# Performance work log

Measured on AMD Instinct MI355X. Metric: run time of the kernel, lower is better.

The kernel has to match this reference:

```python
import jax, jax.numpy as jnp
import numpy as np

SEQ = 32
D = 32  # d_model == GRU hidden size


def _gru_scan(gates_x, w_hh, b_hh):
    """gates_x: [S, B, 3H] precomputed input projections (r,z,n order, PyTorch convention).
    Returns outputs [S, B, H]."""
    H = w_hh.shape[1]
    B = gates_x.shape[1]

    def step(h, gx):
        gh = h @ w_hh.T + b_hh  # [B, 3H]
        r = jax.nn.sigmoid(gx[:, :H] + gh[:, :H])
        z = jax.nn.sigmoid(gx[:, H:2 * H] + gh[:, H:2 * H])
        n = jnp.tanh(gx[:, 2 * H:] + r * gh[:, 2 * H:])
        h_new = (1.0 - z) * n + z * h
        return h_new, h_new

    h0 = jnp.zeros((B, H), gates_x.dtype)
    _, ys = jax.lax.scan(step, h0, gates_x)
    return ys


def setup_inputs() -> dict:
    key = jax.random.key(0)
    ks = jax.random.split(key, 16)
    s = 0.1
    inp = {
        "x": jax.random.normal(ks[0], (32768, SEQ), dtype=jnp.float32),
        # feature extractor: Linear(1,16) -> LeakyReLU -> Linear(16,32)
        "w1": jax.random.normal(ks[1], (16, 1), dtype=jnp.float32) * s,
        "b1": jax.random.normal(ks[2], (16,), dtype=jnp.float32) * s,
        "w2": jax.random.normal(ks[3], (D, 16), dtype=jnp.float32) * s,
        "b2": jax.random.normal(ks[4], (D,), dtype=jnp.float32) * s,
        # GRU forward direction (PyTorch layout: [3H, in], gates r,z,n)
        "w_ih_f": jax.random.normal(ks[5], (3 * D, D), dtype=jnp.float32) * s,
        "w_hh_f": jax.random.normal(ks[6], (3 * D, D), dtype=jnp.float32) * s,
        "b_ih_f": jax.random.normal(ks[7], (3 * D,), dtype=jnp.float32) * s,
        "b_hh_f": jax.random.normal(ks[8], (3 * D,), dtype=jnp.float32) * s,
        # GRU backward direction
        "w_ih_b": jax.random.normal(ks[9], (3 * D, D), dtype=jnp.float32) * s,
        "w_hh_b": jax.random.normal(ks[10], (3 * D, D), dtype=jnp.float32) * s,
        "b_ih_b": jax.random.normal(ks[11], (3 * D,), dtype=jnp.float32) * s,
        "b_hh_b": jax.random.normal(ks[12], (3 * D,), dtype=jnp.float32) * s,
        # decoder: Linear(2*D, 128)
        "w_dec": jax.random.normal(ks[13], (128, 2 * D), dtype=jnp.float32) * s,
        "b_dec": jax.random.normal(ks[14], (128,), dtype=jnp.float32) * s,
    }
    return inp


def reference(x, w1, b1, w2, b2,
              w_ih_f, w_hh_f, b_ih_f, b_hh_f,
              w_ih_b, w_hh_b, b_ih_b, b_hh_b,
              w_dec, b_dec):
    x = x.reshape(-1, SEQ, 1)                      # [B, S, 1]
    h = jax.nn.leaky_relu(x @ w1.T + b1, 0.01)     # [B, S, 16]
    feat = h @ w2.T + b2                           # [B, S, D]

    # forward direction
    gx_f = jnp.einsum('bsd,gd->sbg', feat, w_ih_f) + b_ih_f  # [S, B, 3D]
    out_f = _gru_scan(gx_f, w_hh_f, b_hh_f)                  # [S, B, D]

    # backward direction: scan over time-reversed input, flip outputs back
    feat_rev = feat[:, ::-1, :]
    gx_b = jnp.einsum('bsd,gd->sbg', feat_rev, w_ih_b) + b_ih_b
    out_b = _gru_scan(gx_b, w_hh_b, b_hh_b)[::-1]            # [S, B, D]

    out = jnp.concatenate([out_f, out_b], axis=-1)  # [S, B, 2D]
    pooled = out.mean(axis=0)                       # [B, 2D]
    return pooled @ w_dec.T + b_dec                 # [B, 128]
```

## Files before the change

### kernel.cpp

```cpp
#include <hip/hip_runtime.h>


#define SEQB 32
#define NH   16
#define DH   32

typedef __attribute__((ext_vector_type(4))) float f32x4;
typedef __attribute__((ext_vector_type(8))) short s16x8;
typedef __attribute__((ext_vector_type(4))) unsigned int u32x4;

#define MFMA_B16(a, b, c) __builtin_amdgcn_mfma_f32_16x16x32_bf16((a), (b), (c), 0, 0, 0)

#define OFF_AHI  0u
#define OFF_ALO  12288u
#define OFF_AGX  24576u
#define OFF_ADEC 36864u
#define OFF_WC   53248u
#define OFF_BC   65536u

__device__ __forceinline__ unsigned short bf16_rne(float x) {
    unsigned u = __float_as_uint(x);
    return (unsigned short)((u + 0x7fffu + ((u >> 16) & 1u)) >> 16);
}
__device__ __forceinline__ unsigned pack_hi(unsigned a, unsigned b) {
    return __builtin_amdgcn_perm(a, b, 0x07060302u);
}
__device__ __forceinline__ int kperm(int q, int e) {
    return (e < 4) ? (4 * q + e) : (4 * q + 12 + e);
}

__global__ __launch_bounds__(1024) void gru_precompute_kernel(
    const float* __restrict__ w_ih_f, const float* __restrict__ b_ih_f,
    const float* __restrict__ w_ih_b, const float* __restrict__ b_ih_b,
    const float* __restrict__ w2, const float* __restrict__ b2,
    const float* __restrict__ whh_f, const float* __restrict__ whh_b,
    const float* __restrict__ bhh_f, const float* __restrict__ bhh_b,
    const float* __restrict__ w_dec,
    unsigned char* __restrict__ ws)
{
    const int t = threadIdx.x;
    float* WC = (float*)(ws + OFF_WC);
    float* BC = (float*)(ws + OFF_BC);

    if (t < 192) {
        const int dir = t / 96, g = t % 96;
        const float* wih = dir ? w_ih_b : w_ih_f;
        const float* bih = dir ? b_ih_b : b_ih_f;
        float acc[NH];
#pragma unroll
        for (int m = 0; m < NH; ++m) acc[m] = 0.0f;
        float ab = bih[g];
        for (int d = 0; d < DH; ++d) {
            float wv = wih[g * DH + d];
            ab = fmaf(wv, b2[d], ab);
#pragma unroll
            for (int m = 0; m < NH; ++m) acc[m] = fmaf(wv, w2[d * NH + m], acc[m]);
        }
#pragma unroll
        for (int m = 0; m < NH; ++m) WC[(dir * 96 + g) * NH + m] = acc[m];
        BC[dir * 96 + g] = ab;
    }
    __syncthreads();

    if (t < 768) {
        const int dir = t / 384, r = t % 384, tt = r / 64, l = r % 64;
        const int gate = tt * 16 + (l & 15);
        const int q = l >> 4;
        const float* whh = dir ? whh_b : whh_f;
        const float* bhh = dir ? bhh_b : bhh_f;
        unsigned short h8[8], l8[8], g8[8];
#pragma unroll
        for (int e = 0; e < 8; ++e) {
            const int u = kperm(q, e);
            float w = whh[gate * DH + u];
            unsigned ub = __float_as_uint(w);
            h8[e] = (unsigned short)(ub >> 16);
            l8[e] = bf16_rne(w - __uint_as_float(ub & 0xffff0000u));
            float gxv = (e < 4) ? WC[(dir * 96 + gate) * NH + 4 * q + e] : 0.0f;
            g8[e] = bf16_rne(gxv);
        }
        const float bias = BC[dir * 96 + gate] + ((gate < 64) ? bhh[gate] : 0.0f);
        const unsigned bb = __float_as_uint(bias);
        if (q == 0) g8[4] = (unsigned short)(bb >> 16);
        if (q == 1) g8[4] = bf16_rne(bias - __uint_as_float(bb & 0xffff0000u));

        unsigned short* dh = (unsigned short*)(ws + OFF_AHI + dir * 6144u + tt * 1024u + l * 16u);
        unsigned short* dl = (unsigned short*)(ws + OFF_ALO + dir * 6144u + tt * 1024u + l * 16u);
        unsigned short* dg = (unsigned short*)(ws + OFF_AGX + dir * 6144u + tt * 1024u + l * 16u);
#pragma unroll
        for (int e = 0; e < 8; ++e) { dh[e] = h8[e]; dl[e] = l8[e]; dg[e] = g8[e]; }
    }
    {
        const int kc = t / 512, r = t % 512, tt = r / 64, l = r % 64;
        const int outn = tt * 16 + (l & 15);
        const int q = l >> 4;
        unsigned short* dd = (unsigned short*)(ws + OFF_ADEC + kc * 8192u + tt * 1024u + l * 16u);
#pragma unroll
        for (int e = 0; e < 8; ++e)
            dd[e] = bf16_rne(w_dec[outn * 64 + kperm(q, e) + 32 * kc]);
    }
}

__global__ __launch_bounds__(64, 2) void gru_mfma_kernel(
    const float* __restrict__ x,
    const float* __restrict__ w1, const float* __restrict__ b1,
    const float* __restrict__ bhh_f, const float* __restrict__ bhh_b,
    const unsigned char* __restrict__ ws,
    const float* __restrict__ b_dec,
    float* __restrict__ out)
{
    const int l = threadIdx.x;
    const int n = l & 15;
    const int q = l >> 4;
    const int rowbase = blockIdx.x * 16;
    const float* xr = x + (size_t)(rowbase + n) * SEQB;

    const float4 w1q = *(const float4*)(w1 + 4 * q);
    const float4 b1q = *(const float4*)(b1 + 4 * q);

    float pFL[4], pFH[4], pBL[4], pBH[4];

#pragma unroll 1
    for (int dir = 0; dir < 2; ++dir) {
        const float* bhh = dir ? bhh_b : bhh_f;
        const unsigned char* pAhi = ws + OFF_AHI + dir * 6144u + l * 16u;
        const unsigned char* pAlo = ws + OFF_ALO + dir * 6144u + l * 16u;
        const unsigned char* pAgx = ws + OFF_AGX + dir * 6144u + l * 16u;
        s16x8 Ahi[6], Alo[6], Agx[6];
#pragma unroll
        for (int tt = 0; tt < 6; ++tt) {
            Ahi[tt] = *(const s16x8*)(pAhi + tt * 1024);
            Alo[tt] = *(const s16x8*)(pAlo + tt * 1024);
            Agx[tt] = *(const s16x8*)(pAgx + tt * 1024);
        }
#pragma unroll
        for (int tt = 0; tt < 6; ++tt)
            asm volatile("" : "+v"(Ahi[tt]), "+v"(Alo[tt]), "+v"(Agx[tt]));
        const float4 bn0f = *(const float4*)(bhh + 64 + 4 * q);
        const float4 bn1f = *(const float4*)(bhh + 80 + 4 * q);
        const f32x4 bhn0 = {bn0f.x, bn0f.y, bn0f.z, bn0f.w};
        const f32x4 bhn1 = {bn1f.x, bn1f.y, bn1f.z, bn1f.w};

        float hL[4] = {0, 0, 0, 0}, hH[4] = {0, 0, 0, 0};
        float pL[4] = {0, 0, 0, 0}, pH[4] = {0, 0, 0, 0};

#pragma unroll 1
        for (int blk = 0; blk < 4; ++blk) {
            const int bb = dir ? 3 - blk : blk;
            const float4 xa = *(const float4*)(xr + bb * 8);
            const float4 xb = *(const float4*)(xr + bb * 8 + 4);
            const float raw[8] = {xa.x, xa.y, xa.z, xa.w, xb.x, xb.y, xb.z, xb.w};
            float xs[8];
#pragma unroll
            for (int i = 0; i < 8; ++i) xs[i] = dir ? raw[7 - i] : raw[i];

#pragma unroll
            for (int i = 0; i < 8; ++i) {
                float t0 = fmaf(xs[i], w1q.x, b1q.x); t0 = fmaxf(t0, 0.01f * t0);
                float t1 = fmaf(xs[i], w1q.y, b1q.y); t1 = fmaxf(t1, 0.01f * t1);
                float t2 = fmaf(xs[i], w1q.z, b1q.z); t2 = fmaxf(t2, 0.01f * t2);
                float t3 = fmaf(xs[i], w1q.w, b1q.w); t3 = fmaxf(t3, 0.01f * t3);
                u32x4 ub1;
                ub1.x = pack_hi(__float_as_uint(t1), __float_as_uint(t0));
                ub1.y = pack_hi(__float_as_uint(t3), __float_as_uint(t2));
                ub1.z = 0x00003F80u;
                ub1.w = 0u;
                const s16x8 Bh1 = __builtin_bit_cast(s16x8, ub1);

                unsigned uL0 = __float_as_uint(hL[0]), uL1 = __float_as_uint(hL[1]);
                unsigned uL2 = __float_as_uint(hL[2]), uL3 = __float_as_uint(hL[3]);
                unsigned uH0 = __float_as_uint(hH[0]), uH1 = __float_as_uint(hH[1]);
                unsigned uH2 = __float_as_uint(hH[2]), uH3 = __float_as_uint(hH[3]);
                u32x4 phh;
                phh.x = pack_hi(uL1, uL0); phh.y = pack_hi(uL3, uL2);
                phh.z = pack_hi(uH1, uH0); phh.w = pack_hi(uH3, uH2);
                float lL0 = hL[0] - __uint_as_float(uL0 & 0xffff0000u);
                float lL1 = hL[1] - __uint_as_float(uL1 & 0xffff0000u);
                float lL2 = hL[2] - __uint_as_float(uL2 & 0xffff0000u);
                float lL3 = hL[3] - __uint_as_float(uL3 & 0xffff0000u);
                float lH0 = hH[0] - __uint_as_float(uH0 & 0xffff0000u);
                float lH1 = hH[1] - __uint_as_float(uH1 & 0xffff0000u);
                float lH2 = hH[2] - __uint_as_float(uH2 & 0xffff0000u);
                float lH3 = hH[3] - __uint_as_float(uH3 & 0xffff0000u);
                u32x4 phl;
                phl.x = pack_hi(__float_as_uint(lL1), __float_as_uint(lL0));
                phl.y = pack_hi(__float_as_uint(lL3), __float_as_uint(lL2));
                phl.z = pack_hi(__float_as_uint(lH1), __float_as_uint(lH0));
                phl.w = pack_hi(__float_as_uint(lH3), __float_as_uint(lH2));
                const s16x8 Bhhi = __builtin_bit_cast(s16x8, phh);
                const s16x8 Bhlo = __builtin_bit_cast(s16x8, phl);

                const f32x4 z4 = {0.0f, 0.0f, 0.0f, 0.0f};
                f32x4 a0 = MFMA_B16(Agx[0], Bh1, z4);
                a0 = MFMA_B16(Alo[0], Bhhi, a0); a0 = MFMA_B16(Ahi[0], Bhlo, a0); a0 = MFMA_B16(Ahi[0], Bhhi, a0);
                f32x4 a1 = MFMA_B16(Agx[1], Bh1, z4);
                a1 = MFMA_B16(Alo[1], Bhhi, a1); a1 = MFMA_B16(Ahi[1], Bhlo, a1); a1 = MFMA_B16(Ahi[1], Bhhi, a1);
                f32x4 a2 = MFMA_B16(Agx[2], Bh1, z4);
                a2 = MFMA_B16(Alo[2], Bhhi, a2); a2 = MFMA_B16(Ahi[2], Bhlo, a2); a2 = MFMA_B16(Ahi[2], Bhhi, a2);
                f32x4 a3 = MFMA_B16(Agx[3], Bh1, z4);
                a3 = MFMA_B16(Alo[3], Bhhi, a3); a3 = MFMA_B16(Ahi[3], Bhlo, a3); a3 = MFMA_B16(Ahi[3], Bhhi, a3);
                f32x4 x4a = MFMA_B16(Agx[4], Bh1, z4);
                f32x4 x5a = MFMA_B16(Agx[5], Bh1, z4);
                f32x4 g4 = MFMA_B16(Alo[4], Bhhi, bhn0);
                g4 = MFMA_B16(Ahi[4], Bhlo, g4); g4 = MFMA_B16(Ahi[4], Bhhi, g4);
                f32x4 g5 = MFMA_B16(Alo[5], Bhhi, bhn1);
                g5 = MFMA_B16(Ahi[5], Bhlo, g5); g5 = MFMA_B16(Ahi[5], Bhhi, g5);

#pragma unroll
                for (int rg = 0; rg < 4; ++rg) {
                    float rL = __builtin_amdgcn_rcpf(1.0f + __expf(-a0[rg]));
                    float zL = __builtin_amdgcn_rcpf(1.0f + __expf(-a2[rg]));
                    float tL = fmaf(rL, g4[rg], x4a[rg]);
                    float nL = fmaf(-2.0f, __builtin_amdgcn_rcpf(1.0f + __expf(tL + tL)), 1.0f);
                    hL[rg] = fmaf(zL, hL[rg] - nL, nL);
                    pL[rg] += hL[rg];

                    float rH = __builtin_amdgcn_rcpf(1.0f + __expf(-a1[rg]));
                    float zH = __builtin_amdgcn_rcpf(1.0f + __expf(-a3[rg]));
                    float tH = fmaf(rH, g5[rg], x5a[rg]);
                    float nH = fmaf(-2.0f, __builtin_amdgcn_rcpf(1.0f + __expf(tH + tH)), 1.0f);
                    hH[rg] = fmaf(zH, hH[rg] - nH, nH);
                    pH[rg] += hH[rg];
                }
            }
        }
        if (dir == 0) {
#pragma unroll
            for (int rg = 0; rg < 4; ++rg) { pFL[rg] = pL[rg]; pFH[rg] = pH[rg]; }
        } else {
#pragma unroll
            for (int rg = 0; rg < 4; ++rg) { pBL[rg] = pL[rg]; pBH[rg] = pH[rg]; }
        }
    }

    {
#pragma unroll
        for (int rg = 0; rg < 4; ++rg) {
            pFL[rg] *= 0.03125f; pFH[rg] *= 0.03125f;
            pBL[rg] *= 0.03125f; pBH[rg] *= 0.03125f;
        }
        u32x4 pfh, pfl, pbh, pbl;
        unsigned v0, v1, v2, v3;
        v0 = __float_as_uint(pFL[0]); v1 = __float_as_uint(pFL[1]);
        v2 = __float_as_uint(pFL[2]); v3 = __float_as_uint(pFL[3]);
        pfh.x = pack_hi(v1, v0); pfh.y = pack_hi(v3, v2);
        pfl.x = pack_hi(__float_as_uint(pFL[1] - __uint_as_float(v1 & 0xffff0000u)),
                        __float_as_uint(pFL[0] - __uint_as_float(v0 & 0xffff0000u)));
        pfl.y = pack_hi(__float_as_uint(pFL[3] - __uint_as_float(v3 & 0xffff0000u)),
                        __float_as_uint(pFL[2] - __uint_as_float(v2 & 0xffff0000u)));
        v0 = __float_as_uint(pFH[0]); v1 = __float_as_uint(pFH[1]);
        v2 = __float_as_uint(pFH[2]); v3 = __float_as_uint(pFH[3]);
        pfh.z = pack_hi(v1, v0); pfh.w = pack_hi(v3, v2);
        pfl.z = pack_hi(__float_as_uint(pFH[1] - __uint_as_float(v1 & 0xffff0000u)),
                        __float_as_uint(pFH[0] - __uint_as_float(v0 & 0xffff0000u)));
        pfl.w = pack_hi(__float_as_uint(pFH[3] - __uint_as_float(v3 & 0xffff0000u)),
                        __float_as_uint(pFH[2] - __uint_as_float(v2 & 0xffff0000u)));
        v0 = __float_as_uint(pBL[0]); v1 = __float_as_uint(pBL[1]);
        v2 = __float_as_uint(pBL[2]); v3 = __float_as_uint(pBL[3]);
        pbh.x = pack_hi(v1, v0); pbh.y = pack_hi(v3, v2);
        pbl.x = pack_hi(__float_as_uint(pBL[1] - __uint_as_float(v1 & 0xffff0000u)),
                        __float_as_uint(pBL[0] - __uint_as_float(v0 & 0xffff0000u)));
        pbl.y = pack_hi(__float_as_uint(pBL[3] - __uint_as_float(v3 & 0xffff0000u)),
                        __float_as_uint(pBL[2] - __uint_as_float(v2 & 0xffff0000u)));
        v0 = __float_as_uint(pBH[0]); v1 = __float_as_uint(pBH[1]);
        v2 = __float_as_uint(pBH[2]); v3 = __float_as_uint(pBH[3]);
        pbh.z = pack_hi(v1, v0); pbh.w = pack_hi(v3, v2);
        pbl.z = pack_hi(__float_as_uint(pBH[1] - __uint_as_float(v1 & 0xffff0000u)),
                        __float_as_uint(pBH[0] - __uint_as_float(v0 & 0xffff0000u)));
        pbl.w = pack_hi(__float_as_uint(pBH[3] - __uint_as_float(v3 & 0xffff0000u)),
                        __float_as_uint(pBH[2] - __uint_as_float(v2 & 0xffff0000u)));
        const s16x8 BpFh = __builtin_bit_cast(s16x8, pfh);
        const s16x8 BpFl = __builtin_bit_cast(s16x8, pfl);
        const s16x8 BpBh = __builtin_bit_cast(s16x8, pbh);
        const s16x8 BpBl = __builtin_bit_cast(s16x8, pbl);

#pragma unroll
        for (int tt = 0; tt < 8; ++tt) {
            const s16x8 A0 = *(const s16x8*)(ws + OFF_ADEC + tt * 1024u + l * 16u);
            const s16x8 A1 = *(const s16x8*)(ws + OFF_ADEC + 8192u + tt * 1024u + l * 16u);
            const float4 bd = *(const float4*)(b_dec + tt * 16 + 4 * q);
            f32x4 acc = {bd.x, bd.y, bd.z, bd.w};
            acc = MFMA_B16(A0, BpFl, acc);
            acc = MFMA_B16(A1, BpBl, acc);
            acc = MFMA_B16(A0, BpFh, acc);
            acc = MFMA_B16(A1, BpBh, acc);
            *(float4*)(out + (size_t)(rowbase + n) * 128 + tt * 16 + 4 * q) =
                make_float4(acc[0], acc[1], acc[2], acc[3]);
        }
    }
}

extern "C" void kernel_launch(void* const* d_in, const int* in_sizes, int n_in,
                              void* d_out, int out_size, void* d_ws, size_t ws_size,
                              hipStream_t stream)
{
    const float* x    = (const float*)d_in[0];
    const float* w1   = (const float*)d_in[1];
    const float* b1   = (const float*)d_in[2];
    const float* w2   = (const float*)d_in[3];
    const float* b2   = (const float*)d_in[4];
    const float* wihf = (const float*)d_in[5];
    const float* whhf = (const float*)d_in[6];
    const float* bihf = (const float*)d_in[7];
    const float* bhhf = (const float*)d_in[8];
    const float* wihb = (const float*)d_in[9];
    const float* whhb = (const float*)d_in[10];
    const float* bihb = (const float*)d_in[11];
    const float* bhhb = (const float*)d_in[12];
    const float* wdec = (const float*)d_in[13];
    const float* bdec = (const float*)d_in[14];
    float* out = (float*)d_out;
    unsigned char* ws = (unsigned char*)d_ws;

    const int B = in_sizes[0] / SEQB;
    const int grid = B / 16;

    hipLaunchKernelGGL(gru_precompute_kernel, dim3(1), dim3(1024), 0, stream,
                       wihf, bihf, wihb, bihb, w2, b2, whhf, whhb, bhhf, bhhb, wdec, ws);
    hipLaunchKernelGGL(gru_mfma_kernel, dim3(grid), dim3(64), 0, stream,
                       x, w1, b1, bhhf, bhhb, ws, bdec, out);
}
```

Measured before the change: 82.59 us.

## Run forward and backward GRU directions in parallel wavefronts with LDS exchange

Each block now has two wavefronts, one per GRU direction, instead of one wavefront running both directions one after the other. The pooled states are exchanged through shared memory after a barrier, and each wave computes half of the decoder output tiles. This halves the serial recurrence chain per block and doubles the wave count, aiming to hide the latency-bound scan. The cost is a small LDS buffer, a block-level sync, and different launch bounds that may constrain register allocation.

New measurement: 274.1 us. +231.9%, slower.

```diff
diff --git a/kernel.cpp b/kernel.cpp
--- a/kernel.cpp
+++ b/kernel.cpp
@@ -101,7 +101,7 @@
     }
 }
 
-__global__ __launch_bounds__(64, 2) void gru_mfma_kernel(
+__global__ __launch_bounds__(128, 4) void gru_mfma_kernel(
     const float* __restrict__ x,
     const float* __restrict__ w1, const float* __restrict__ b1,
     const float* __restrict__ bhh_f, const float* __restrict__ bhh_b,
@@ -109,7 +109,11 @@
     const float* __restrict__ b_dec,
     float* __restrict__ out)
 {
-    const int l = threadIdx.x;
+    __shared__ __align__(16) u32x4 lds_comb[2][64][2];
+
+    const int tid = threadIdx.x;
+    const int dir = tid >> 6;
+    const int l   = tid & 63;
     const int n = l & 15;
     const int q = l >> 4;
     const int rowbase = blockIdx.x * 16;
@@ -118,172 +122,157 @@
     const float4 w1q = *(const float4*)(w1 + 4 * q);
     const float4 b1q = *(const float4*)(b1 + 4 * q);
 
-    float pFL[4], pFH[4], pBL[4], pBH[4];
+    const float* bhh = dir ? bhh_b : bhh_f;
+    const unsigned char* pAhi = ws + OFF_AHI + dir * 6144u + l * 16u;
+    const unsigned char* pAlo = ws + OFF_ALO + dir * 6144u + l * 16u;
+    const unsigned char* pAgx = ws + OFF_AGX + dir * 6144u + l * 16u;
+    s16x8 Ahi[6], Alo[6], Agx[6];
+#pragma unroll
+    for (int tt = 0; tt < 6; ++tt) {
+        Ahi[tt] = *(const s16x8*)(pAhi + tt * 1024);
+        Alo[tt] = *(const s16x8*)(pAlo + tt * 1024);
+        Agx[tt] = *(const s16x8*)(pAgx + tt * 1024);
+    }
+#pragma unroll
+    for (int tt = 0; tt < 6; ++tt)
+        asm volatile("" : "+v"(Ahi[tt]), "+v"(Alo[tt]), "+v"(Agx[tt]));
+    const float4 bn0f = *(const float4*)(bhh + 64 + 4 * q);
+    const float4 bn1f = *(const float4*)(bhh + 80 + 4 * q);
+    const f32x4 bhn0 = {bn0f.x, bn0f.y, bn0f.z, bn0f.w};
+    const f32x4 bhn1 = {bn1f.x, bn1f.y, bn1f.z, bn1f.w};
+
+    float hL[4] = {0, 0, 0, 0}, hH[4] = {0, 0, 0, 0};
+    float pL[4] = {0, 0, 0, 0}, pH[4] = {0, 0, 0, 0};
 
 #pragma unroll 1
-    for (int dir = 0; dir < 2; ++dir) {
-        const float* bhh = dir ? bhh_b : bhh_f;
-        const unsigned char* pAhi = ws + OFF_AHI + dir * 6144u + l * 16u;
-        const unsigned char* pAlo = ws + OFF_ALO + dir * 6144u + l * 16u;
-        const unsigned char* pAgx = ws + OFF_AGX + dir * 6144u + l * 16u;
-        s16x8 Ahi[6], Alo[6], Agx[6];
-#pragma unroll
-        for (int tt = 0; tt < 6; ++tt) {
-            Ahi[tt] = *(const s16x8*)(pAhi + tt * 1024);
-            Alo[tt] = *(const s16x8*)(pAlo + tt * 1024);
-            Agx[tt] = *(const s16x8*)(pAgx + tt * 1024);
-        }
-#pragma unroll
-        for (int tt = 0; tt < 6; ++tt)
-            asm volatile("" : "+v"(Ahi[tt]), "+v"(Alo[tt]), "+v"(Agx[tt]));
-        const float4 bn0f = *(const float4*)(bhh + 64 + 4 * q);
-        const float4 bn1f = *(const float4*)(bhh + 80 + 4 * q);
-        const f32x4 bhn0 = {bn0f.x, bn0f.y, bn0f.z, bn0f.w};
-        const f32x4 bhn1 = {bn1f.x, bn1f.y, bn1f.z, bn1f.w};
-
-        float hL[4] = {0, 0, 0, 0}, hH[4] = {0, 0, 0, 0};
-        float pL[4] = {0, 0, 0, 0}, pH[4] = {0, 0, 0, 0};
-
-#pragma unroll 1
-        for (int blk = 0; blk < 4; ++blk) {
-            const int bb = dir ? 3 - blk : blk;
-            const float4 xa = *(const float4*)(xr + bb * 8);
-            const float4 xb = *(const float4*)(xr + bb * 8 + 4);
-            const float raw[8] = {xa.x, xa.y, xa.z, xa.w, xb.x, xb.y, xb.z, xb.w};
-            float xs[8];
-#pragma unroll
-            for (int i = 0; i < 8; ++i) xs[i] = dir ? raw[7 - i] : raw[i];
-
-#pragma unroll
-            for (int i = 0; i < 8; ++i) {
-                float t0 = fmaf(xs[i], w1q.x, b1q.x); t0 = fmaxf(t0, 0.01f * t0);
-                float t1 = fmaf(xs[i], w1q.y, b1q.y); t1 = fmaxf(t1, 0.01f * t1);
-                float t2 = fmaf(xs[i], w1q.z, b1q.z); t2 = fmaxf(t2, 0.01f * t2);
-                float t3 = fmaf(xs[i], w1q.w, b1q.w); t3 = fmaxf(t3, 0.01f * t3);
-                u32x4 ub1;
-                ub1.x = pack_hi(__float_as_uint(t1), __float_as_uint(t0));
-                ub1.y = pack_hi(__float_as_uint(t3), __float_as_uint(t2));
-                ub1.z = 0x00003F80u;
-                ub1.w = 0u;
-                const s16x8 Bh1 = __builtin_bit_cast(s16x8, ub1);
-
-                unsigned uL0 = __float_as_uint(hL[0]), uL1 = __float_as_uint(hL[1]);
-                unsigned uL2 = __float_as_uint(hL[2]), uL3 = __float_as_uint(hL[3]);
-                unsigned uH0 = __float_as_uint(hH[0]), uH1 = __float_as_uint(hH[1]);
-                unsigned uH2 = __float_as_uint(hH[2]), uH3 = __float_as_uint(hH[3]);
-                u32x4 phh;
-                phh.x = pack_hi(uL1, uL0); phh.y = pack_hi(uL3, uL2);
-                phh.z = pack_hi(uH1, uH0); phh.w = pack_hi(uH3, uH2);
-                float lL0 = hL[0] - __uint_as_float(uL0 & 0xffff0000u);
-                float lL1 = hL[1] - __uint_as_float(uL1 & 0xffff0000u);
-                float lL2 = hL[2] - __uint_as_float(uL2 & 0xffff0000u);
-                float lL3 = hL[3] - __uint_as_float(uL3 & 0xffff0000u);
-                float lH0 = hH[0] - __uint_as_float(uH0 & 0xffff0000u);
-                float lH1 = hH[1] - __uint_as_float(uH1 & 0xffff0000u);
-                float lH2 = hH[2] - __uint_as_float(uH2 & 0xffff0000u);
-                float lH3 = hH[3] - __uint_as_float(uH3 & 0xffff0000u);
-                u32x4 phl;
-                phl.x = pack_hi(__float_as_uint(lL1), __float_as_uint(lL0));
-                phl.y = pack_hi(__float_as_uint(lL3), __float_as_uint(lL2));
-                phl.z = pack_hi(__float_as_uint(lH1), __float_as_uint(lH0));
-                phl.w = pack_hi(__float_as_uint(lH3), __float_as_uint(lH2));
-                const s16x8 Bhhi = __builtin_bit_cast(s16x8, phh);
-                const s16x8 Bhlo = __builtin_bit_cast(s16x8, phl);
-
-                const f32x4 z4 = {0.0f, 0.0f, 0.0f, 0.0f};
-                f32x4 a0 = MFMA_B16(Agx[0], Bh1, z4);
-                a0 = MFMA_B16(Alo[0], Bhhi, a0); a0 = MFMA_B16(Ahi[0], Bhlo, a0); a0 = MFMA_B16(Ahi[0], Bhhi, a0);
-                f32x4 a1 = MFMA_B16(Agx[1], Bh1, z4);
-                a1 = MFMA_B16(Alo[1], Bhhi, a1); a1 = MFMA_B16(Ahi[1], Bhlo, a1); a1 = MFMA_B16(Ahi[1], Bhhi, a1);
-                f32x4 a2 = MFMA_B16(Agx[2], Bh1, z4);
-                a2 = MFMA_B16(Alo[2], Bhhi, a2); a2 = MFMA_B16(Ahi[2], Bhlo, a2); a2 = MFMA_B16(Ahi[2], Bhhi, a2);
-                f32x4 a3 = MFMA_B16(Agx[3], Bh1, z4);
-                a3 = MFMA_B16(Alo[3], Bhhi, a3); a3 = MFMA_B16(Ahi[3], Bhlo, a3); a3 = MFMA_B16(Ahi[3], Bhhi, a3);
-                f32x4 x4a = MFMA_B16(Agx[4], Bh1, z4);
-                f32x4 x5a = MFMA_B16(Agx[5], Bh1, z4);
-                f32x4 g4 = MFMA_B16(Alo[4], Bhhi, bhn0);
-                g4 = MFMA_B16(Ahi[4], Bhlo, g4); g4 = MFMA_B16(Ahi[4], Bhhi, g4);
-                f32x4 g5 = MFMA_B16(Alo[5], Bhhi, bhn1);
-                g5 = MFMA_B16(Ahi[5], Bhlo, g5); g5 = MFMA_B16(Ahi[5], Bhhi, g5);
-
-#pragma unroll
-                for (int rg = 0; rg < 4; ++rg) {
-                    float rL = __builtin_amdgcn_rcpf(1.0f + __expf(-a0[rg]));
-                    float zL = __builtin_amdgcn_rcpf(1.0f + __expf(-a2[rg]));
-                    float tL = fmaf(rL, g4[rg], x4a[rg]);
-                    float nL = fmaf(-2.0f, __builtin_amdgcn_rcpf(1.0f + __expf(tL + tL)), 1.0f);
-                    hL[rg] = fmaf(zL, hL[rg] - nL, nL);
-                    pL[rg] += hL[rg];
-
-                    float rH = __builtin_amdgcn_rcpf(1.0f + __expf(-a1[rg]));
-                    float zH = __builtin_amdgcn_rcpf(1.0f + __expf(-a3[rg]));
-                    float tH = fmaf(rH, g5[rg], x5a[rg]);
-                    float nH = fmaf(-2.0f, __builtin_amdgcn_rcpf(1.0f + __expf(tH + tH)), 1.0f);
-                    hH[rg] = fmaf(zH, hH[rg] - nH, nH);
-                    pH[rg] += hH[rg];
-                }
+    for (int blk = 0; blk < 4; ++blk) {
+        const int bb = dir ? 3 - blk : blk;
+        const float4 xa = *(const float4*)(xr + bb * 8);
+        const float4 xb = *(const float4*)(xr + bb * 8 + 4);
+        float xs[8] = {xa.x, xa.y, xa.z, xa.w, xb.x, xb.y, xb.z, xb.w};
+        if (dir) {
+            float r0 = xs[0], r1 = xs[1], r2 = xs[2], r3 = xs[3];
+            xs[0] = xs[7]; xs[1] = xs[6]; xs[2] = xs[5]; xs[3] = xs[4];
+            xs[4] = r3; xs[5] = r2; xs[6] = r1; xs[7] = r0;
+        }
+
+#pragma unroll
+        for (int i = 0; i < 8; ++i) {
+            float t0 = fmaf(xs[i], w1q.x, b1q.x); t0 = fmaxf(t0, 0.01f * t0);
+            float t1 = fmaf(xs[i], w1q.y, b1q.y); t1 = fmaxf(t1, 0.01f * t1);
+            float t2 = fmaf(xs[i], w1q.z, b1q.z); t2 = fmaxf(t2, 0.01f * t2);
+            float t3 = fmaf(xs[i], w1q.w, b1q.w); t3 = fmaxf(t3, 0.01f * t3);
+            u32x4 ub1;
+            ub1.x = pack_hi(__float_as_uint(t1), __float_as_uint(t0));
+            ub1.y = pack_hi(__float_as_uint(t3), __float_as_uint(t2));
+            ub1.z = 0x00003F80u;
+            ub1.w = 0u;
+            const s16x8 Bh1 = __builtin_bit_cast(s16x8, ub1);
+
+            unsigned uL0 = __float_as_uint(hL[0]), uL1 = __float_as_uint(hL[1]);
+            unsigned uL2 = __float_as_uint(hL[2]), uL3 = __float_as_uint(hL[3]);
+            unsigned uH0 = __float_as_uint(hH[0]), uH1 = __float_as_uint(hH[1]);
+            unsigned uH2 = __float_as_uint(hH[2]), uH3 = __float_as_uint(hH[3]);
+            u32x4 phh;
+            phh.x = pack_hi(uL1, uL0); phh.y = pack_hi(uL3, uL2);
+            phh.z = pack_hi(uH1, uH0); phh.w = pack_hi(uH3, uH2);
+            float lL0 = hL[0] - __uint_as_float(uL0 & 0xffff0000u);
+            float lL1 = hL[1] - __uint_as_float(uL1 & 0xffff0000u);
+            float lL2 = hL[2] - __uint_as_float(uL2 & 0xffff0000u);
+            float lL3 = hL[3] - __uint_as_float(uL3 & 0xffff0000u);
+            float lH0 = hH[0] - __uint_as_float(uH0 & 0xffff0000u);
+            float lH1 = hH[1] - __uint_as_float(uH1 & 0xffff0000u);
+            float lH2 = hH[2] - __uint_as_float(uH2 & 0xffff0000u);
+            float lH3 = hH[3] - __uint_as_float(uH3 & 0xffff0000u);
+            u32x4 phl;
+            phl.x = pack_hi(__float_as_uint(lL1), __float_as_uint(lL0));
+            phl.y = pack_hi(__float_as_uint(lL3), __float_as_uint(lL2));
+            phl.z = pack_hi(__float_as_uint(lH1), __float_as_uint(lH0));
+            phl.w = pack_hi(__float_as_uint(lH3), __float_as_uint(lH2));
+            const s16x8 Bhhi = __builtin_bit_cast(s16x8, phh);
+            const s16x8 Bhlo = __builtin_bit_cast(s16x8, phl);
+
+            const f32x4 z4 = {0.0f, 0.0f, 0.0f, 0.0f};
+            f32x4 a0 = MFMA_B16(Agx[0], Bh1, z4);
+            a0 = MFMA_B16(Alo[0], Bhhi, a0); a0 = MFMA_B16(Ahi[0], Bhlo, a0); a0 = MFMA_B16(Ahi[0], Bhhi, a0);
+            f32x4 a1 = MFMA_B16(Agx[1], Bh1, z4);
+            a1 = MFMA_B16(Alo[1], Bhhi, a1); a1 = MFMA_B16(Ahi[1], Bhlo, a1); a1 = MFMA_B16(Ahi[1], Bhhi, a1);
+            f32x4 a2 = MFMA_B16(Agx[2], Bh1, z4);
+            a2 = MFMA_B16(Alo[2], Bhhi, a2); a2 = MFMA_B16(Ahi[2], Bhlo, a2); a2 = MFMA_B16(Ahi[2], Bhhi, a2);
+            f32x4 a3 = MFMA_B16(Agx[3], Bh1, z4);
+            a3 = MFMA_B16(Alo[3], Bhhi, a3); a3 = MFMA_B16(Ahi[3], Bhlo, a3); a3 = MFMA_B16(Ahi[3], Bhhi, a3);
+            f32x4 x4a = MFMA_B16(Agx[4], Bh1, z4);
+            f32x4 x5a = MFMA_B16(Agx[5], Bh1, z4);
+            f32x4 g4 = MFMA_B16(Alo[4], Bhhi, bhn0);
+            g4 = MFMA_B16(Ahi[4], Bhlo, g4); g4 = MFMA_B16(Ahi[4], Bhhi, g4);
+            f32x4 g5 = MFMA_B16(Alo[5], Bhhi, bhn1);
+            g5 = MFMA_B16(Ahi[5], Bhlo, g5); g5 = MFMA_B16(Ahi[5], Bhhi, g5);
+
+#pragma unroll
+            for (int rg = 0; rg < 4; ++rg) {
+                float rL = __builtin_amdgcn_rcpf(1.0f + __expf(-a0[rg]));
+                float zL = __builtin_amdgcn_rcpf(1.0f + __expf(-a2[rg]));
+                float tL = fmaf(rL, g4[rg], x4a[rg]);
+                float nL = fmaf(-2.0f, __builtin_amdgcn_rcpf(1.0f + __expf(tL + tL)), 1.0f);
+                hL[rg] = fmaf(zL, hL[rg] - nL, nL);
+                pL[rg] += hL[rg];
+
+                float rH = __builtin_amdgcn_rcpf(1.0f + __expf(-a1[rg]));
+                float zH = __builtin_amdgcn_rcpf(1.0f + __expf(-a3[rg]));
+                float tH = fmaf(rH, g5[rg], x5a[rg]);
+                float nH = fmaf(-2.0f, __builtin_amdgcn_rcpf(1.0f + __expf(tH + tH)), 1.0f);
+                hH[rg] = fmaf(zH, hH[rg] - nH, nH);
+                pH[rg] += hH[rg];
             }
         }
+    }
+
+    {
+#pragma unroll
+        for (int rg = 0; rg < 4; ++rg) { pL[rg] *= 0.03125f; pH[rg] *= 0.03125f; }
+        unsigned v0, v1, v2, v3;
+        u32x4 ph, pl;
+        v0 = __float_as_uint(pL[0]); v1 = __float_as_uint(pL[1]);
+        v2 = __float_as_uint(pL[2]); v3 = __float_as_uint(pL[3]);
+        ph.x = pack_hi(v1, v0); ph.y = pack_hi(v3, v2);
+        pl.x = pack_hi(__float_as_uint(pL[1] - __uint_as_float(v1 & 0xffff0000u)),
+                       __float_as_uint(pL[0] - __uint_as_float(v0 & 0xffff0000u)));
+        pl.y = pack_hi(__float_as_uint(pL[3] - __uint_as_float(v3 & 0xffff0000u)),
+                       __float_as_uint(pL[2] - __uint_as_float(v2 & 0xffff0000u)));
+        v0 = __float_as_uint(pH[0]); v1 = __float_as_uint(pH[1]);
+        v2 = __float_as_uint(pH[2]); v3 = __float_as_uint(pH[3]);
+        ph.z = pack_hi(v1, v0); ph.w = pack_hi(v3, v2);
+        pl.z = pack_hi(__float_as_uint(pH[1] - __uint_as_float(v1 & 0xffff0000u)),
+                       __float_as_uint(pH[0] - __uint_as_float(v0 & 0xffff0000u)));
+        pl.w = pack_hi(__float_as_uint(pH[3] - __uint_as_float(v3 & 0xffff0000u)),
+                       __float_as_uint(pH[2] - __uint_as_float(v2 & 0xffff0000u)));
+
+        lds_comb[dir][l][0] = ph;
+        lds_comb[dir][l][1] = pl;
+        __syncthreads();
+        const u32x4 oh = lds_comb[dir ^ 1][l][0];
+        const u32x4 ol = lds_comb[dir ^ 1][l][1];
+
+        s16x8 BFh, BFl, BBh, BBl;
         if (dir == 0) {
-#pragma unroll
-            for (int rg = 0; rg < 4; ++rg) { pFL[rg] = pL[rg]; pFH[rg] = pH[rg]; }
+            BFh = __builtin_bit_cast(s16x8, ph); BFl = __builtin_bit_cast(s16x8, pl);
+            BBh = __builtin_bit_cast(s16x8, oh); BBl = __builtin_bit_cast(s16x8, ol);
         } else {
-#pragma unroll
-            for (int rg = 0; rg < 4; ++rg) { pBL[rg] = pL[rg]; pBH[rg] = pH[rg]; }
-        }
-    }
-
-    {
-#pragma unroll
-        for (int rg = 0; rg < 4; ++rg) {
-            pFL[rg] *= 0.03125f; pFH[rg] *= 0.03125f;
-            pBL[rg] *= 0.03125f; pBH[rg] *= 0.03125f;
-        }
-        u32x4 pfh, pfl, pbh, pbl;
-        unsigned v0, v1, v2, v3;
-        v0 = __float_as_uint(pFL[0]); v1 = __float_as_uint(pFL[1]);
-        v2 = __float_as_uint(pFL[2]); v3 = __float_as_uint(pFL[3]);
-        pfh.x = pack_hi(v1, v0); pfh.y = pack_hi(v3, v2);
-        pfl.x = pack_hi(__float_as_uint(pFL[1] - __uint_as_float(v1 & 0xffff0000u)),
-                        __float_as_uint(pFL[0] - __uint_as_float(v0 & 0xffff0000u)));
-        pfl.y = pack_hi(__float_as_uint(pFL[3] - __uint_as_float(v3 & 0xffff0000u)),
-                        __float_as_uint(pFL[2] - __uint_as_float(v2 & 0xffff0000u)));
-        v0 = __float_as_uint(pFH[0]); v1 = __float_as_uint(pFH[1]);
-        v2 = __float_as_uint(pFH[2]); v3 = __float_as_uint(pFH[3]);
-        pfh.z = pack_hi(v1, v0); pfh.w = pack_hi(v3, v2);
-        pfl.z = pack_hi(__float_as_uint(pFH[1] - __uint_as_float(v1 & 0xffff0000u)),
-                        __float_as_uint(pFH[0] - __uint_as_float(v0 & 0xffff0000u)));
-        pfl.w = pack_hi(__float_as_uint(pFH[3] - __uint_as_float(v3 & 0xffff0000u)),
-                        __float_as_uint(pFH[2] - __uint_as_float(v2 & 0xffff0000u)));
-        v0 = __float_as_uint(pBL[0]); v1 = __float_as_uint(pBL[1]);
-        v2 = __float_as_uint(pBL[2]); v3 = __float_as_uint(pBL[3]);
-        pbh.x = pack_hi(v1, v0); pbh.y = pack_hi(v3, v2);
-        pbl.x = pack_hi(__float_as_uint(pBL[1] - __uint_as_float(v1 & 0xffff0000u)),
-                        __float_as_uint(pBL[0] - __uint_as_float(v0 & 0xffff0000u)));
-        pbl.y = pack_hi(__float_as_uint(pBL[3] - __uint_as_float(v3 & 0xffff0000u)),
-                        __float_as_uint(pBL[2] - __uint_as_float(v2 & 0xffff0000u)));
-        v0 = __float_as_uint(pBH[0]); v1 = __float_as_uint(pBH[1]);
-        v2 = __float_as_uint(pBH[2]); v3 = __float_as_uint(pBH[3]);
-        pbh.z = pack_hi(v1, v0); pbh.w = pack_hi(v3, v2);
-        pbl.z = pack_hi(__float_as_uint(pBH[1] - __uint_as_float(v1 & 0xffff0000u)),
-                        __float_as_uint(pBH[0] - __uint_as_float(v0 & 0xffff0000u)));
-        pbl.w = pack_hi(__float_as_uint(pBH[3] - __uint_as_float(v3 & 0xffff0000u)),
-                        __float_as_uint(pBH[2] - __uint_as_float(v2 & 0xffff0000u)));
-        const s16x8 BpFh = __builtin_bit_cast(s16x8, pfh);
-        const s16x8 BpFl = __builtin_bit_cast(s16x8, pfl);
-        const s16x8 BpBh = __builtin_bit_cast(s16x8, pbh);
-        const s16x8 BpBl = __builtin_bit_cast(s16x8, pbl);
-
-#pragma unroll
-        for (int tt = 0; tt < 8; ++tt) {
+            BFh = __builtin_bit_cast(s16x8, oh); BFl = __builtin_bit_cast(s16x8, ol);
+            BBh = __builtin_bit_cast(s16x8, ph); BBl = __builtin_bit_cast(s16x8, pl);
+        }
+
+#pragma unroll
+        for (int ti = 0; ti < 4; ++ti) {
+            const int tt = dir * 4 + ti;
             const s16x8 A0 = *(const s16x8*)(ws + OFF_ADEC + tt * 1024u + l * 16u);
             const s16x8 A1 = *(const s16x8*)(ws + OFF_ADEC + 8192u + tt * 1024u + l * 16u);
             const float4 bd = *(const float4*)(b_dec + tt * 16 + 4 * q);
             f32x4 acc = {bd.x, bd.y, bd.z, bd.w};
-            acc = MFMA_B16(A0, BpFl, acc);
-            acc = MFMA_B16(A1, BpBl, acc);
-            acc = MFMA_B16(A0, BpFh, acc);
-            acc = MFMA_B16(A1, BpBh, acc);
+            acc = MFMA_B16(A0, BFl, acc);
+            acc = MFMA_B16(A1, BBl, acc);
+            acc = MFMA_B16(A0, BFh, acc);
+            acc = MFMA_B16(A1, BBh, acc);
             *(float4*)(out + (size_t)(rowbase + n) * 128 + tt * 16 + 4 * q) =
                 make_float4(acc[0], acc[1], acc[2], acc[3]);
         }
@@ -317,6 +306,6 @@
 
     hipLaunchKernelGGL(gru_precompute_kernel, dim3(1), dim3(1024), 0, stream,
                        wihf, bihf, wihb, bihb, w2, b2, whhf, whhb, bhhf, bhhb, wdec, ws);
-    hipLaunchKernelGGL(gru_mfma_kernel, dim3(grid), dim3(64), 0, stream,
+    hipLaunchKernelGGL(gru_mfma_kernel, dim3(grid), dim3(128), 0, stream,
                        x, w1, b1, bhhf, bhhb, ws, bdec, out);
 }
```
